# Kernel optimization log

Hardware: AMD Instinct MI355X
Metric: run time of the kernel (lower is better)

The kernel has to match this reference:

```python
import jax, jax.numpy as jnp
import numpy as np


def _tconv(x, w, b):
    # x: [B,C_in,N,T], w: [C_out,C_in,1,k] -> 'same' padding along T only
    pad = (w.shape[-1] - 1) // 2
    y = jax.lax.conv_general_dilated(x, w, (1, 1), [(0, 0), (pad, pad)],
                                     dimension_numbers=('NCHW', 'OIHW', 'NCHW'))
    return y + b[None, :, None, None]


def _temporal(x, w1, b1, w2, b2, w3, b3):
    # x: [B,T,N,C] -> gated GLU-style temporal conv -> [B,T,N,C_out]
    xc = jnp.transpose(x, (0, 3, 2, 1))  # [B,C,N,T]
    p = _tconv(xc, w1, b1)
    q = jax.nn.sigmoid(_tconv(xc, w2, b2))
    h = jax.nn.relu(p * q + _tconv(xc, w3, b3))
    return jnp.transpose(h, (0, 3, 2, 1))


def _cheb(x, src, dst, wn, W, bias):
    # x: [M,N,C]; scaled Laplacian with lambda_max=2 => L_hat = -D^-1/2 A D^-1/2
    # (diag +1 from L and -1 self-loop fill cancel exactly, as in PyG ChebConv)
    N = x.shape[1]

    def spmv(v):
        msgs = v[:, src, :] * wn[None, :, None]
        return jnp.zeros_like(v).at[:, dst, :].add(msgs)

    Tx0 = x
    out = jnp.einsum('mnc,cd->mnd', Tx0, W[0])
    Tx1 = spmv(Tx0)
    out = out + jnp.einsum('mnc,cd->mnd', Tx1, W[1])
    Txp, Txpp = Tx1, Tx0
    for k in range(2, W.shape[0]):
        Txk = 2.0 * spmv(Txp) - Txpp
        out = out + jnp.einsum('mnc,cd->mnd', Txk, W[k])
        Txpp, Txp = Txp, Txk
    return out + bias


def _bn_train(out, gamma, beta, eps=1e-5):
    # BatchNorm2d in training mode (batch stats, biased variance) over [B,C,N,T]
    ob = jnp.transpose(out, (0, 3, 2, 1))
    mu = jnp.mean(ob, axis=(0, 2, 3), keepdims=True)
    var = jnp.mean((ob - mu) ** 2, axis=(0, 2, 3), keepdims=True)
    ob = (ob - mu) * jax.lax.rsqrt(var + eps)
    ob = ob * gamma[None, :, None, None] + beta[None, :, None, None]
    return jnp.transpose(ob, (0, 3, 2, 1))


def setup_inputs():
    B, T, N, Cin, H, k, K, E = 16, 12, 4096, 2, 64, 3, 3, 65536
    ks = jax.random.split(jax.random.key(0), 20)
    sc = 0.1
    return {
        'x': jax.random.normal(ks[0], (B, T, N, Cin), jnp.float32),
        'edge_index': jax.random.randint(ks[1], (2, E), 0, N),
        'edge_attr': jax.random.uniform(ks[2], (E,), jnp.float32),
        't1_w1': jax.random.normal(ks[3], (H, Cin, 1, k), jnp.float32) * sc,
        't1_b1': jnp.zeros((H,), jnp.float32),
        't1_w2': jax.random.normal(ks[4], (H, Cin, 1, k), jnp.float32) * sc,
        't1_b2': jnp.zeros((H,), jnp.float32),
        't1_w3': jax.random.normal(ks[5], (H, Cin, 1, k), jnp.float32) * sc,
        't1_b3': jnp.zeros((H,), jnp.float32),
        'cheb_W': jax.random.normal(ks[6], (K, H, H), jnp.float32) * sc,
        'cheb_b': jnp.zeros((H,), jnp.float32),
        't2_w1': jax.random.normal(ks[7], (H, H, 1, k), jnp.float32) * sc,
        't2_b1': jnp.zeros((H,), jnp.float32),
        't2_w2': jax.random.normal(ks[8], (H, H, 1, k), jnp.float32) * sc,
        't2_b2': jnp.zeros((H,), jnp.float32),
        't2_w3': jax.random.normal(ks[9], (H, H, 1, k), jnp.float32) * sc,
        't2_b3': jnp.zeros((H,), jnp.float32),
        'bn_g': jnp.ones((H,), jnp.float32),
        'bn_b': jnp.zeros((H,), jnp.float32),
    }


def reference(x, edge_index, edge_attr,
              t1_w1, t1_b1, t1_w2, t1_b2, t1_w3, t1_b3,
              cheb_W, cheb_b,
              t2_w1, t2_b1, t2_w2, t2_b2, t2_w3, t2_b3,
              bn_g, bn_b):
    t1 = _temporal(x, t1_w1, t1_b1, t1_w2, t1_b2, t1_w3, t1_b3)  # [B,T,N,H]
    B, T, N, C = t1.shape
    src, dst = edge_index[0], edge_index[1]
    # sym normalization: deg from source scatter; -D^-1/2 w D^-1/2 edge weights
    deg = jnp.zeros((N,), t1.dtype).at[src].add(edge_attr)
    safe = jnp.where(deg > 0, deg, 1.0)
    dis = jnp.where(deg > 0, jax.lax.rsqrt(safe), 0.0)
    wn = -dis[src] * edge_attr * dis[dst]
    g = _cheb(t1.reshape(B * T, N, C), src, dst, wn, cheb_W, cheb_b)
    g = jax.nn.relu(g).reshape(B, T, N, C)
    out = _temporal(g, t2_w1, t2_b1, t2_w2, t2_b2, t2_w3, t2_b3)
    return _bn_train(out, bn_g, bn_b)
```

## Files before the change

kernel.cpp:

```cpp
#include <hip/hip_runtime.h>
#include <stdint.h>

#define BB 16
#define TT 12
#define NN 4096
#define HH 64
#define EE 65536
#define MM (BB*TT)
#define ROWS (MM*NN)
#define TOT (ROWS*HH)
#define NBUCKET 256
#define T2_GRID 2048
#define T2_NT 6

typedef __attribute__((ext_vector_type(8))) __bf16 bf16x8;
typedef __attribute__((ext_vector_type(8))) unsigned short us8;
typedef __attribute__((ext_vector_type(4))) float f32x4;
typedef __attribute__((ext_vector_type(2))) unsigned int ui2;

__device__ __forceinline__ unsigned short f2bf(float f){
  unsigned u = __builtin_bit_cast(unsigned, f);
  u += 0x7fffu + ((u >> 16) & 1u);
  return (unsigned short)(u >> 16);
}
__device__ __forceinline__ float bf2f(unsigned short s){
  unsigned u = ((unsigned)s) << 16;
  return __builtin_bit_cast(float, u);
}
__device__ __forceinline__ float lo2f(unsigned v){ return __builtin_bit_cast(float, v << 16); }
__device__ __forceinline__ float hi2f(unsigned v){ return __builtin_bit_cast(float, v & 0xffff0000u); }
__device__ __forceinline__ bf16x8 ldbf8(const unsigned short* p){
  us8 u = *reinterpret_cast<const us8*>(p);
  return __builtin_bit_cast(bf16x8, u);
}


__global__ void k_deg_cnt(const int* __restrict__ src, const int* __restrict__ dst,
                          const float* __restrict__ attr,
                          float* __restrict__ deg, int* __restrict__ cnt){
  int e = blockIdx.x * 256 + threadIdx.x;
  if (e < EE){
    atomicAdd(&deg[src[e]], attr[e]);
    atomicAdd(&cnt[dst[e]], 1);
  }
}

__global__ void k_wn(const int* __restrict__ src, const int* __restrict__ dst,
                     const float* __restrict__ attr, const float* __restrict__ deg,
                     float* __restrict__ wn){
  int e = blockIdx.x * 256 + threadIdx.x;
  if (e < EE){
    float ds = deg[src[e]], dd = deg[dst[e]];
    float rs = ds > 0.f ? rsqrtf(ds) : 0.f;
    float rd = dd > 0.f ? rsqrtf(dd) : 0.f;
    wn[e] = -rs * attr[e] * rd;
  }
}

__global__ void k_scan(const int* __restrict__ cnt, int* __restrict__ rowptr,
                       int* __restrict__ fill){
  __shared__ int lds[1024];
  int t = threadIdx.x;
  int c0 = cnt[4*t], c1 = cnt[4*t+1], c2 = cnt[4*t+2], c3 = cnt[4*t+3];
  int s = c0 + c1 + c2 + c3;
  lds[t] = s; __syncthreads();
  for (int off = 1; off < 1024; off <<= 1){
    int v = (t >= off) ? lds[t-off] : 0;
    __syncthreads();
    lds[t] += v;
    __syncthreads();
  }
  int excl = lds[t] - s;
  rowptr[4*t]   = excl;            fill[4*t]   = excl;
  rowptr[4*t+1] = excl + c0;       fill[4*t+1] = excl + c0;
  rowptr[4*t+2] = excl + c0 + c1;  fill[4*t+2] = excl + c0 + c1;
  rowptr[4*t+3] = excl + c0+c1+c2; fill[4*t+3] = excl + c0+c1+c2;
  if (t == 1023) rowptr[4096] = lds[1023];
}

__global__ void k_csr(const int* __restrict__ dst, const int* __restrict__ src,
                      const float* __restrict__ wn, int* __restrict__ fill,
                      ui2* __restrict__ csre){
  int e = blockIdx.x * 256 + threadIdx.x;
  if (e < EE){
    int d = dst[e];
    int pos = atomicAdd(&fill[d], 1);
    ui2 mw;
    mw.x = (unsigned)src[e];
    mw.y = __builtin_bit_cast(unsigned, wn[e]);
    csre[pos] = mw;
  }
}


__global__ void k_wprep(const float* __restrict__ chebW,
                        const float* __restrict__ w1, const float* __restrict__ w2,
                        const float* __restrict__ w3,
                        const float* __restrict__ e1w, const float* __restrict__ e1b,
                        const float* __restrict__ e2w, const float* __restrict__ e2b,
                        const float* __restrict__ e3w, const float* __restrict__ e3b,
                        unsigned short* __restrict__ wfD, unsigned short* __restrict__ wfF,
                        unsigned short* __restrict__ wfE){
  int gt = blockIdx.x * blockDim.x + threadIdx.x;
  int stride = gridDim.x * blockDim.x;
  for (int i = gt; i < 12288; i += stride){
    int kl = i & 31, cc = (i >> 5) & 63, mk = i >> 11;
    int kt = mk & 1, mat = mk >> 1;
    int k = kt * 32 + kl;
    float v;
    if (mat == 0)      v = chebW[k*64 + cc] - chebW[2*4096 + k*64 + cc];
    else if (mat == 1) v = chebW[4096 + k*64 + cc];
    else               v = 2.f * chebW[2*4096 + k*64 + cc];
    wfD[i] = f2bf(v);
  }
  for (int i = gt; i < 36864; i += stride){
    int kl = i & 31, hh = (i >> 5) & 63, ck = i >> 11;
    int kt = ck % 6, conv = ck / 6;
    int k = kt * 32 + kl, dt = k >> 6, ci = k & 63;
    const float* w = (conv == 0) ? w1 : ((conv == 1) ? w2 : w3);
    wfF[i] = f2bf(w[(hh*64 + ci)*3 + dt]);
  }
  for (int i = gt; i < 6144; i += stride){
    int k = i & 31, hh = (i >> 5) & 63, conv = i >> 11;
    const float* w = (conv == 0) ? e1w : ((conv == 1) ? e2w : e3w);
    const float* b = (conv == 0) ? e1b : ((conv == 1) ? e2b : e3b);
    float v = 0.f;
    if (k < 6)       v = w[(hh*2 + (k & 1))*3 + (k >> 1)];
    else if (k == 6) v = b[hh];
    wfE[i] = f2bf(v);
  }
}


__global__ __launch_bounds__(256) void k_temporal1(
    const float* __restrict__ x, const unsigned short* __restrict__ wfE,
    unsigned short* __restrict__ U){
  const int tid = threadIdx.x;
  const int wv = tid >> 6, lane = tid & 63;
  const int lhi = lane >> 4, llo = lane & 15;
  const int blk = blockIdx.x;
  const int bt = blk >> 6, nb = blk & 63;
  const int t = bt - (bt / TT) * TT;

  us8 au = {0,0,0,0,0,0,0,0};
  if (lhi == 0){
    const int n = nb*64 + wv*16 + llo;
    #pragma unroll
    for (int dt = 0; dt < 3; ++dt){
      int tp = t + dt - 1;
      if (tp >= 0 && tp < TT){
        const float2 v = *reinterpret_cast<const float2*>(
            x + ((size_t)(bt + dt - 1) * NN + n) * 2);
        if (dt == 0){ au[0] = f2bf(v.x); au[1] = f2bf(v.y); }
        if (dt == 1){ au[2] = f2bf(v.x); au[3] = f2bf(v.y); }
        if (dt == 2){ au[4] = f2bf(v.x); au[5] = f2bf(v.y); }
      }
    }
    au[6] = 0x3f80;
  }
  const bf16x8 af = __builtin_bit_cast(bf16x8, au);

  const f32x4 z = {0.f, 0.f, 0.f, 0.f};
  f32x4 acc[3][4];
  #pragma unroll
  for (int conv = 0; conv < 3; ++conv)
    #pragma unroll
    for (int ht = 0; ht < 4; ++ht){
      bf16x8 bw = ldbf8(wfE + (size_t)((conv*64) + ht*16 + llo)*32 + lhi*8);
      acc[conv][ht] = __builtin_amdgcn_mfma_f32_16x16x32_bf16(af, bw, z, 0, 0, 0);
    }

  #pragma unroll
  for (int ht = 0; ht < 4; ++ht){
    const int h = ht*16 + llo;
    #pragma unroll
    for (int i = 0; i < 4; ++i){
      float p = acc[0][ht][i];
      float q = acc[1][ht][i];
      float r = acc[2][ht][i];
      float sig = 1.f / (1.f + __expf(-q));
      float o = fmaxf(fmaf(p, sig, r), 0.f);
      const int n = nb*64 + wv*16 + lhi*4 + i;
      U[((size_t)n * MM + bt) * 64 + h] = f2bf(o);
    }
  }
}


__global__ __launch_bounds__(256) void k_fused_sc(
    const unsigned short* __restrict__ U,
    const int* __restrict__ rowptr, const ui2* __restrict__ csre,
    const unsigned short* __restrict__ wfD, const float* __restrict__ cheb_b,
    unsigned short* __restrict__ G0bf, unsigned short* __restrict__ P){
  __shared__ unsigned short vlds[4096];
  const int tid = threadIdx.x;
  int blk = blockIdx.x;
  blk = (blk & 7) * 1536 + (blk >> 3);
  const int mg = blk >> 8;
  const int ng = blk & 255;
  const int wv = tid >> 6, lane = tid & 63;
  const int p = lane >> 4, c4 = lane & 15;
  const int loff = p*64 + c4*4;

  const unsigned short* Umg = U + (size_t)mg * 256;

  #pragma unroll
  for (int j = 0; j < 4; ++j){
    const int n = ng*16 + wv*4 + j;
    const int e0 = __builtin_amdgcn_readfirstlane(rowptr[n]);
    const int e1 = __builtin_amdgcn_readfirstlane(rowptr[n+1]);
    float a0 = 0.f, a1 = 0.f, a2 = 0.f, a3 = 0.f;
    for (int e = e0; e < e1; e += 8){
      int ss[8]; float ww[8];
      #pragma unroll
      for (int u = 0; u < 8; ++u){
        const int ee = e + u;
        const bool in = ee < e1;
        const ui2 mw = csre[in ? ee : e0];
        ss[u] = (int)__builtin_amdgcn_readfirstlane(mw.x);
        const float wvv = __builtin_bit_cast(float, __builtin_amdgcn_readfirstlane(mw.y));
        ww[u] = in ? wvv : 0.f;
      }
      ui2 d[8];
      #pragma unroll
      for (int u = 0; u < 8; ++u)
        d[u] = *reinterpret_cast<const ui2*>(Umg + (size_t)ss[u] * 12288 + loff);
      #pragma unroll
      for (int u = 0; u < 8; ++u){
        const float w = ww[u];
        a0 = fmaf(w, lo2f(d[u].x), a0);
        a1 = fmaf(w, hi2f(d[u].x), a1);
        a2 = fmaf(w, lo2f(d[u].y), a2);
        a3 = fmaf(w, hi2f(d[u].y), a3);
      }
    }
    const int r = (wv*4 + j)*4 + p;
    const int byteoff = r*128 + ((c4*8) ^ ((r & 7) << 4));
    ushort4 pk;
    pk.x = f2bf(a0); pk.y = f2bf(a1); pk.z = f2bf(a2); pk.w = f2bf(a3);
    *reinterpret_cast<ushort4*>(reinterpret_cast<char*>(vlds) + byteoff) = pk;
  }
  __syncthreads();

  const int lhi = lane >> 4, llo = lane & 15;
  const int c = wv * 16 + llo;

  bf16x8 bA[2], bW1[2], bW2[2];
  #pragma unroll
  for (int kt = 0; kt < 2; ++kt){
    bA[kt]  = ldbf8(wfD + (size_t)((0*2 + kt)*64 + c)*32 + lhi*8);
    bW1[kt] = ldbf8(wfD + (size_t)((1*2 + kt)*64 + c)*32 + lhi*8);
    bW2[kt] = ldbf8(wfD + (size_t)((2*2 + kt)*64 + c)*32 + lhi*8);
  }
  const f32x4 z = {0.f, 0.f, 0.f, 0.f};
  f32x4 accG[4], accP[4];
  #pragma unroll
  for (int rt = 0; rt < 4; ++rt){ accG[rt] = z; accP[rt] = z; }

  #pragma unroll
  for (int rt = 0; rt < 4; ++rt){
    const int m = rt*16 + llo;
    const size_t gr = ((size_t)(ng*16 + (m >> 2))) * MM + mg*4 + (m & 3);
    const unsigned short* up = U + gr*64 + lhi*8;
    #pragma unroll
    for (int kt = 0; kt < 2; ++kt){
      bf16x8 au = ldbf8(up + kt*32);
      const int vboff = m*128 + (((kt*64) + lhi*16) ^ ((m & 7) << 4));
      bf16x8 av = __builtin_bit_cast(bf16x8, *reinterpret_cast<const us8*>(
          reinterpret_cast<const char*>(vlds) + vboff));
      accG[rt] = __builtin_amdgcn_mfma_f32_16x16x32_bf16(au, bA[kt],  accG[rt], 0, 0, 0);
      accG[rt] = __builtin_amdgcn_mfma_f32_16x16x32_bf16(av, bW1[kt], accG[rt], 0, 0, 0);
      accP[rt] = __builtin_amdgcn_mfma_f32_16x16x32_bf16(av, bW2[kt], accP[rt], 0, 0, 0);
    }
  }
  const float bias = cheb_b[c];
  #pragma unroll
  for (int rt = 0; rt < 4; ++rt){
    #pragma unroll
    for (int i = 0; i < 4; ++i){
      const int mrow = rt*16 + lhi*4 + i;
      const size_t gr = ((size_t)(ng*16 + (mrow >> 2))) * MM + mg*4 + (mrow & 3);
      G0bf[gr*64 + c] = f2bf(accG[rt][i] + bias);
      P[gr*64 + c]    = f2bf(accP[rt][i]);
    }
  }
}


__global__ __launch_bounds__(256) void k_spmv2(
    const unsigned short* __restrict__ X,
    const int* __restrict__ rowptr,
    const ui2* __restrict__ csre,
    const unsigned short* __restrict__ G0bf,
    unsigned short* __restrict__ Y){
  constexpr int EU = 16;
  const int nb = gridDim.x;
  int bs = (blockIdx.x & 7) * (nb >> 3) + (blockIdx.x >> 3);
  int wg = bs * 4 + (threadIdx.x >> 6);
  wg = __builtin_amdgcn_readfirstlane(wg);
  const int lane = threadIdx.x & 63;
  const int mg = wg >> 12, n = wg & (NN-1);
  const int e0 = __builtin_amdgcn_readfirstlane(rowptr[n]);
  const int e1 = __builtin_amdgcn_readfirstlane(rowptr[n+1]);
  const unsigned short* Xmg = X + (size_t)mg * 256;
  const int loff = lane * 4;

  float a0 = 0.f, a1 = 0.f, a2 = 0.f, a3 = 0.f;

  for (int e = e0; e < e1; e += EU){
    int ss[EU]; float ww[EU];
    #pragma unroll
    for (int u = 0; u < EU; ++u){
      const int ee = e + u;
      const bool in = ee < e1;
      const ui2 mw = csre[in ? ee : e0];
      ss[u] = (int)__builtin_amdgcn_readfirstlane(mw.x);
      const float wv = __builtin_bit_cast(float, __builtin_amdgcn_readfirstlane(mw.y));
      ww[u] = in ? wv : 0.f;
    }
    ui2 d[EU];
    #pragma unroll
    for (int u = 0; u < EU; ++u)
      d[u] = *reinterpret_cast<const ui2*>(Xmg + (size_t)ss[u] * 12288 + loff);
    #pragma unroll
    for (int u = 0; u < EU; ++u){
      const float w = ww[u];
      a0 = fmaf(w, lo2f(d[u].x), a0);
      a1 = fmaf(w, hi2f(d[u].x), a1);
      a2 = fmaf(w, lo2f(d[u].y), a2);
      a3 = fmaf(w, hi2f(d[u].y), a3);
    }
  }

  const size_t oidx = (size_t)n * 12288 + mg * 256 + loff;
  {
    ui2 gd = *reinterpret_cast<const ui2*>(G0bf + oidx);
    a0 = fmaxf(a0 + lo2f(gd.x), 0.f);
    a1 = fmaxf(a1 + hi2f(gd.x), 0.f);
    a2 = fmaxf(a2 + lo2f(gd.y), 0.f);
    a3 = fmaxf(a3 + hi2f(gd.y), 0.f);
  }
  ui2 o;
  o.x = (unsigned)f2bf(a0) | ((unsigned)f2bf(a1) << 16);
  o.y = (unsigned)f2bf(a2) | ((unsigned)f2bf(a3) << 16);
  *reinterpret_cast<ui2*>(Y + oidx) = o;
}


__device__ __forceinline__ void t2_load(const unsigned short* __restrict__ g,
                                        int tile, int tid, uint4* st){
  const int bt = tile >> 6, nb = tile & 63;
  const int t = bt - (bt / TT) * TT;
  #pragma unroll
  for (int j = 0; j < 6; ++j){
    const int plane = j >> 1;
    const int tp = t + plane - 1;
    const int idx = ((j & 1) << 8) + tid;
    const int row = idx >> 3;
    const int innerb = (idx & 7) * 16;
    if (tp >= 0 && tp < TT){
      const unsigned short* sp = g
          + ((size_t)(nb*64 + row) * MM + (bt + plane - 1)) * 64
          + ((innerb ^ ((row & 7) << 4)) >> 1);
      st[j] = *reinterpret_cast<const uint4*>(sp);
    } else {
      st[j] = make_uint4(0u, 0u, 0u, 0u);
    }
  }
}

__global__ __launch_bounds__(256, 2) void k_temporal2(
    const unsigned short* __restrict__ g,
    const unsigned short* __restrict__ wfF,
    const float* __restrict__ b1, const float* __restrict__ b2, const float* __restrict__ b3,
    unsigned short* __restrict__ obf, float* __restrict__ bnstat2){
  __shared__ unsigned short smem[2][12288];
  const int tid = threadIdx.x;
  const int wv = tid >> 6, lane = tid & 63;
  const int lhi = lane >> 4, llo = lane & 15;
  const int h = wv * 16 + llo;
  const int h0 = wv * 16 + lhi * 4;

  bf16x8 bw[3][6];
  #pragma unroll
  for (int cv = 0; cv < 3; ++cv)
    #pragma unroll
    for (int kt = 0; kt < 6; ++kt)
      bw[cv][kt] = ldbf8(wfF + (size_t)((cv*6 + kt)*64 + h)*32 + lhi*8);

  const f32x4 vb1 = *reinterpret_cast<const f32x4*>(b1 + h0);
  const f32x4 vb2 = *reinterpret_cast<const f32x4*>(b2 + h0);
  const f32x4 vb3 = *reinterpret_cast<const f32x4*>(b3 + h0);
  const f32x4 z = {0.f, 0.f, 0.f, 0.f};

  uint4 st[6];
  t2_load(g, blockIdx.x, tid, st);
  #pragma unroll
  for (int j = 0; j < 6; ++j)
    *reinterpret_cast<uint4*>(&smem[0][(size_t)(j*256 + tid) * 8]) = st[j];
  __syncthreads();

  int cur = 0;
  for (int it = 0; it < T2_NT; ++it){
    const int tile = blockIdx.x + it * T2_GRID;
    const int bt = tile >> 6, nb = tile & 63;

    if (it + 1 < T2_NT)
      t2_load(g, tile + T2_GRID, tid, st);

    const unsigned short* sb = smem[cur];
    f32x4 acc[3][4];
    #pragma unroll
    for (int cv = 0; cv < 3; ++cv)
      #pragma unroll
      for (int rt = 0; rt < 4; ++rt) acc[cv][rt] = z;

    #pragma unroll
    for (int kt = 0; kt < 6; ++kt){
      const int dt = kt >> 1;
      const int qb = (kt & 1) * 64 + lhi * 16;
      #pragma unroll
      for (int rt = 0; rt < 4; ++rt){
        const int row = rt*16 + llo;
        bf16x8 a = __builtin_bit_cast(bf16x8, *reinterpret_cast<const us8*>(
            sb + dt*4096 + row*64 + ((qb ^ ((row & 7) << 4)) >> 1)));
        acc[0][rt] = __builtin_amdgcn_mfma_f32_16x16x32_bf16(bw[0][kt], a, acc[0][rt], 0, 0, 0);
        acc[1][rt] = __builtin_amdgcn_mfma_f32_16x16x32_bf16(bw[1][kt], a, acc[1][rt], 0, 0, 0);
        acc[2][rt] = __builtin_amdgcn_mfma_f32_16x16x32_bf16(bw[2][kt], a, acc[2][rt], 0, 0, 0);
      }
    }

    f32x4 lsum = z, lsq = z;
    #pragma unroll
    for (int rt = 0; rt < 4; ++rt){
      const int n = nb*64 + rt*16 + llo;
      ushort4 pk;
      unsigned short* pp = reinterpret_cast<unsigned short*>(&pk);
      #pragma unroll
      for (int i = 0; i < 4; ++i){
        float p = acc[0][rt][i] + vb1[i];
        float q = acc[1][rt][i] + vb2[i];
        float r = acc[2][rt][i] + vb3[i];
        float sig = 1.f / (1.f + __expf(-q));
        float o = fmaxf(fmaf(p, sig, r), 0.f);
        pp[i] = f2bf(o);
        lsum[i] += o; lsq[i] = fmaf(o, o, lsq[i]);
      }
      *reinterpret_cast<ushort4*>(&obf[((size_t)bt * NN + n) * 64 + h0]) = pk;
    }
    #pragma unroll
    for (int m = 1; m < 16; m <<= 1){
      #pragma unroll
      for (int i = 0; i < 4; ++i){
        lsum[i] += __shfl_xor(lsum[i], m);
        lsq[i]  += __shfl_xor(lsq[i], m);
      }
    }
    if (llo == 0){
      float* bs = bnstat2 + (size_t)(tile & (NBUCKET-1)) * 128;
      #pragma unroll
      for (int i = 0; i < 4; ++i){
        atomicAdd(&bs[h0 + i], lsum[i]);
        atomicAdd(&bs[64 + h0 + i], lsq[i]);
      }
    }

    if (it + 1 < T2_NT){
      #pragma unroll
      for (int j = 0; j < 6; ++j)
        *reinterpret_cast<uint4*>(&smem[cur ^ 1][(size_t)(j*256 + tid) * 8]) = st[j];
      __syncthreads();
      cur ^= 1;
    }
  }
}


__global__ void k_bnfinal(const float* __restrict__ bnstat2, float* __restrict__ bnstat){
  int t = threadIdx.x;
  float s = 0.f;
  for (int b = 0; b < NBUCKET; ++b) s += bnstat2[(size_t)b * 128 + t];
  bnstat[t] = s;
}

__global__ __launch_bounds__(256) void k_bnapply(
    const unsigned short* __restrict__ obf, float* __restrict__ out,
    const float* __restrict__ bnstat,
    const float* __restrict__ gamma, const float* __restrict__ beta){
  __shared__ float ssc[64], sfb[64];
  int tid = threadIdx.x;
  if (tid < 64){
    const float inv = 1.f / (float)ROWS;
    float s = bnstat[tid], q = bnstat[64 + tid];
    float mu = s * inv;
    float var = q * inv - mu * mu;
    if (var < 0.f) var = 0.f;
    float sc = gamma[tid] * rsqrtf(var + 1e-5f);
    ssc[tid] = sc;
    sfb[tid] = beta[tid] - mu * sc;
  }
  __syncthreads();
  const int ngrp = TOT / 8;
  for (int i = blockIdx.x * 256 + tid; i < ngrp; i += gridDim.x * 256){
    us8 v = *reinterpret_cast<const us8*>(obf + (size_t)i * 8);
    const int c0 = (i * 8) & 63;
    f32x4 lo, hi;
    #pragma unroll
    for (int j = 0; j < 4; ++j)
      lo[j] = fmaf(bf2f(v[j]), ssc[c0 + j], sfb[c0 + j]);
    #pragma unroll
    for (int j = 0; j < 4; ++j)
      hi[j] = fmaf(bf2f(v[4 + j]), ssc[c0 + 4 + j], sfb[c0 + 4 + j]);
    *reinterpret_cast<f32x4*>(out + (size_t)i * 8)     = lo;
    *reinterpret_cast<f32x4*>(out + (size_t)i * 8 + 4) = hi;
  }
}


extern "C" void kernel_launch(void* const* d_in, const int* in_sizes, int n_in,
                              void* d_out, int out_size, void* d_ws, size_t ws_size,
                              hipStream_t stream){
  const float* x     = (const float*)d_in[0];
  const int*   ei    = (const int*)d_in[1];
  const float* attr  = (const float*)d_in[2];
  const float* t1w1  = (const float*)d_in[3];
  const float* t1b1  = (const float*)d_in[4];
  const float* t1w2  = (const float*)d_in[5];
  const float* t1b2  = (const float*)d_in[6];
  const float* t1w3  = (const float*)d_in[7];
  const float* t1b3  = (const float*)d_in[8];
  const float* chebW = (const float*)d_in[9];
  const float* chebB = (const float*)d_in[10];
  const float* t2w1  = (const float*)d_in[11];
  const float* t2b1  = (const float*)d_in[12];
  const float* t2w2  = (const float*)d_in[13];
  const float* t2b2  = (const float*)d_in[14];
  const float* t2w3  = (const float*)d_in[15];
  const float* t2b3  = (const float*)d_in[16];
  const float* bng   = (const float*)d_in[17];
  const float* bnb   = (const float*)d_in[18];
  const int* src = ei;
  const int* dst = ei + EE;

  const size_t SZ_U = (size_t)ROWS * 64 * 2;
  char* ws = (char*)d_ws;
  unsigned short* bufA = (unsigned short*)ws;
  unsigned short* bufB = (unsigned short*)(ws + SZ_U);
  size_t off = 2 * SZ_U;
  float* deg    = (float*)(ws + off); off += 4096 * 4;
  int*   cnt    = (int*)(ws + off);   off += 4096 * 4;
  int*   rowptr = (int*)(ws + off);   off += 4128 * 4;
  int*   fill   = (int*)(ws + off);   off += 4096 * 4;
  float* wn     = (float*)(ws + off); off += EE * 4;
  ui2*   csre   = (ui2*)(ws + off);   off += EE * 8;
  unsigned short* wfD = (unsigned short*)(ws + off); off += 12288 * 2;
  unsigned short* wfF = (unsigned short*)(ws + off); off += 36864 * 2;
  unsigned short* wfE = (unsigned short*)(ws + off); off += 6144 * 2;
  float* bnstat = (float*)(ws + off); off += 128 * 4;
  float* bnstat2 = (float*)(ws + off); off += NBUCKET * 128 * 4;

  unsigned short* G0bf = (unsigned short*)d_out;

  hipMemsetAsync(deg, 0, 4096 * 4, stream);
  hipMemsetAsync(cnt, 0, 4096 * 4, stream);
  hipMemsetAsync(bnstat2, 0, NBUCKET * 128 * 4, stream);

  k_deg_cnt<<<EE/256, 256, 0, stream>>>(src, dst, attr, deg, cnt);
  k_wn<<<EE/256, 256, 0, stream>>>(src, dst, attr, deg, wn);
  k_scan<<<1, 1024, 0, stream>>>(cnt, rowptr, fill);
  k_csr<<<EE/256, 256, 0, stream>>>(dst, src, wn, fill, csre);
  k_wprep<<<64, 256, 0, stream>>>(chebW, t2w1, t2w2, t2w3,
                                  t1w1, t1b1, t1w2, t1b2, t1w3, t1b3,
                                  wfD, wfF, wfE);

  k_temporal1<<<ROWS/64, 256, 0, stream>>>(x, wfE, bufA );
  k_fused_sc<<<ROWS/64, 256, 0, stream>>>(bufA , rowptr, csre, wfD, chebB,
                                          G0bf, bufB );
  k_spmv2<<<(MM/4)*NN/4, 256, 0, stream>>>(bufB , rowptr, csre, G0bf, bufA );
  k_temporal2<<<T2_GRID, 256, 0, stream>>>(bufA , wfF, t2b1, t2b2, t2b3,
                                           bufB , bnstat2);
  k_bnfinal<<<1, 128, 0, stream>>>(bnstat2, bnstat);
  k_bnapply<<<2048, 256, 0, stream>>>(bufB , (float*)d_out, bnstat, bng, bnb);
}
```

Before: 640.1 us.

## Make each wave own its own rows in fused SpMV+MFMA kernel, dropping block barrier

```diff
diff --git a/kernel.cpp b/kernel.cpp
--- a/kernel.cpp
+++ b/kernel.cpp
@@ -203,8 +203,8 @@
   const int loff = p*64 + c4*4;
 
   const unsigned short* Umg = U + (size_t)mg * 256;
-
-  #pragma unroll
+  char* wq = reinterpret_cast<char*>(vlds) + wv*2048;
+
   for (int j = 0; j < 4; ++j){
     const int n = ng*16 + wv*4 + j;
     const int e0 = __builtin_amdgcn_readfirstlane(rowptr[n]);
@@ -234,54 +234,44 @@
         a3 = fmaf(w, hi2f(d[u].y), a3);
       }
     }
-    const int r = (wv*4 + j)*4 + p;
+    const int r = j*4 + p;
     const int byteoff = r*128 + ((c4*8) ^ ((r & 7) << 4));
     ushort4 pk;
     pk.x = f2bf(a0); pk.y = f2bf(a1); pk.z = f2bf(a2); pk.w = f2bf(a3);
-    *reinterpret_cast<ushort4*>(reinterpret_cast<char*>(vlds) + byteoff) = pk;
-  }
-  __syncthreads();
+    *reinterpret_cast<ushort4*>(wq + byteoff) = pk;
+  }
 
   const int lhi = lane >> 4, llo = lane & 15;
-  const int c = wv * 16 + llo;
-
-  bf16x8 bA[2], bW1[2], bW2[2];
+  const size_t grA = ((size_t)(ng*16 + wv*4 + (llo >> 2))) * MM + mg*4 + (llo & 3);
+  const unsigned short* up = U + grA*64 + lhi*8;
+  bf16x8 au[2], av[2];
   #pragma unroll
   for (int kt = 0; kt < 2; ++kt){
-    bA[kt]  = ldbf8(wfD + (size_t)((0*2 + kt)*64 + c)*32 + lhi*8);
-    bW1[kt] = ldbf8(wfD + (size_t)((1*2 + kt)*64 + c)*32 + lhi*8);
-    bW2[kt] = ldbf8(wfD + (size_t)((2*2 + kt)*64 + c)*32 + lhi*8);
+    au[kt] = ldbf8(up + kt*32);
+    const int vboff = llo*128 + (((kt*64) + lhi*16) ^ ((llo & 7) << 4));
+    av[kt] = __builtin_bit_cast(bf16x8, *reinterpret_cast<const us8*>(wq + vboff));
   }
   const f32x4 z = {0.f, 0.f, 0.f, 0.f};
-  f32x4 accG[4], accP[4];
-  #pragma unroll
-  for (int rt = 0; rt < 4; ++rt){ accG[rt] = z; accP[rt] = z; }
-
-  #pragma unroll
-  for (int rt = 0; rt < 4; ++rt){
-    const int m = rt*16 + llo;
-    const size_t gr = ((size_t)(ng*16 + (m >> 2))) * MM + mg*4 + (m & 3);
-    const unsigned short* up = U + gr*64 + lhi*8;
+  #pragma unroll
+  for (int ct = 0; ct < 4; ++ct){
+    const int c = ct*16 + llo;
+    f32x4 accG = z, accP = z;
     #pragma unroll
     for (int kt = 0; kt < 2; ++kt){
-      bf16x8 au = ldbf8(up + kt*32);
-      const int vboff = m*128 + (((kt*64) + lhi*16) ^ ((m & 7) << 4));
-      bf16x8 av = __builtin_bit_cast(bf16x8, *reinterpret_cast<const us8*>(
-          reinterpret_cast<const char*>(vlds) + vboff));
-      accG[rt] = __builtin_amdgcn_mfma_f32_16x16x32_bf16(au, bA[kt],  accG[rt], 0, 0, 0);
-      accG[rt] = __builtin_amdgcn_mfma_f32_16x16x32_bf16(av, bW1[kt], accG[rt], 0, 0, 0);
-      accP[rt] = __builtin_amdgcn_mfma_f32_16x16x32_bf16(av, bW2[kt], accP[rt], 0, 0, 0);
-    }
-  }
-  const float bias = cheb_b[c];
-  #pragma unroll
-  for (int rt = 0; rt < 4; ++rt){
+      bf16x8 bA  = ldbf8(wfD + (size_t)((0*2 + kt)*64 + c)*32 + lhi*8);
+      bf16x8 bW1 = ldbf8(wfD + (size_t)((1*2 + kt)*64 + c)*32 + lhi*8);
+      bf16x8 bW2 = ldbf8(wfD + (size_t)((2*2 + kt)*64 + c)*32 + lhi*8);
+      accG = __builtin_amdgcn_mfma_f32_16x16x32_bf16(au[kt], bA,  accG, 0, 0, 0);
+      accG = __builtin_amdgcn_mfma_f32_16x16x32_bf16(av[kt], bW1, accG, 0, 0, 0);
+      accP = __builtin_amdgcn_mfma_f32_16x16x32_bf16(av[kt], bW2, accP, 0, 0, 0);
+    }
+    const float bias = cheb_b[c];
     #pragma unroll
     for (int i = 0; i < 4; ++i){
-      const int mrow = rt*16 + lhi*4 + i;
-      const size_t gr = ((size_t)(ng*16 + (mrow >> 2))) * MM + mg*4 + (mrow & 3);
-      G0bf[gr*64 + c] = f2bf(accG[rt][i] + bias);
-      P[gr*64 + c]    = f2bf(accP[rt][i]);
+      const int rl = lhi*4 + i;
+      const size_t gr = ((size_t)(ng*16 + wv*4 + (rl >> 2))) * MM + mg*4 + (rl & 3);
+      G0bf[gr*64 + c] = f2bf(accG[i] + bias);
+      P[gr*64 + c]    = f2bf(accP[i]);
     }
   }
 }
```

After: 675.4 us. 1.06x slower.
